# Performance work log

Hardware: AMD Instinct MI355X
Metric: run time of the kernel (lower is better)

Reference implementation:

```python
import jax, jax.numpy as jnp
import numpy as np

N_HEADS = 8
EPS = 1e-6


def setup_inputs() -> dict:
    key = jax.random.key(0)
    k1, k2, k3, k4, k5 = jax.random.split(key, 5)
    C_in, C_out = 512, 512
    x = jax.random.normal(k1, (4, C_in, 128, 128), dtype=jnp.float32)
    # Linear layers: torch stores weight as (out, in); init ~ U(-1/sqrt(in), 1/sqrt(in))
    s_in = 1.0 / np.sqrt(C_in)
    w_qkv = jax.random.uniform(k2, (3 * C_in, C_in), minval=-s_in, maxval=s_in, dtype=jnp.float32)
    b_qkv = jax.random.uniform(k3, (3 * C_in,), minval=-s_in, maxval=s_in, dtype=jnp.float32)
    w_out = jax.random.uniform(k4, (C_out, C_in), minval=-s_in, maxval=s_in, dtype=jnp.float32)
    b_out = jax.random.uniform(k5, (C_out,), minval=-s_in, maxval=s_in, dtype=jnp.float32)
    return {"x": x, "w_qkv": w_qkv, "b_qkv": b_qkv, "w_out": w_out, "b_out": b_out}


def reference(x, w_qkv, b_qkv, w_out, b_out):
    B, C = x.shape[0], x.shape[1]
    spatial = x.shape[2:]
    c = C // N_HEADS  # channels per head
    # features_last=False: move channels to last, flatten spatial -> (B, N, C)
    xl = jnp.moveaxis(x, 1, -1).reshape(B, -1, C)
    N = xl.shape[1]
    qkv = xl @ w_qkv.T + b_qkv  # (B, N, 3*C)
    # einops '(qkv head channels)': qkv outermost, then head, then channels
    qkv = qkv.reshape(B, N, 3, N_HEADS, c)
    q = jax.nn.relu(qkv[:, :, 0])  # (B, N, H, c)
    k = jax.nn.relu(qkv[:, :, 1])
    v = qkv[:, :, 2]
    # Associativity: value @ key^T @ query == value @ (key^T @ query).
    # kq[b,h,c,d] = sum_n k[b,n,h,c] * q[b,n,h,d]  -> small (c x c) per head
    kq = jnp.einsum('bnhc,bnhd->bhcd', k, q)
    vkq = jnp.einsum('bnhc,bhcd->bnhd', v, kq)  # (B, N, H, c)
    # Padded ones-row of value corresponds to column-sum of kq over axis c
    norm = kq.sum(axis=2)[:, None] + EPS  # (B, 1, H, c)
    attn = vkq / norm  # (B, N, H, c)
    # torch: (B,H,N,c).moveaxis(1,-1) -> (B,N,c,H); flatten(-2) -> (B,N,c*H)
    attn = jnp.transpose(attn, (0, 1, 3, 2)).reshape(B, N, -1)
    out = attn @ w_out.T + b_out  # (B, N, C_out)
    out = out.reshape(B, *spatial, -1)
    out = jnp.moveaxis(out, -1, 1)  # (B, C_out, *spatial)
    return out
```

## Files before the change

### kernel.cpp

```cpp
#include <hip/hip_runtime.h>
#include <hip/hip_bf16.h>
#include <stdint.h>

#define NSP 16384
#define BATCH 4
#define EPSV 1e-6f

typedef __attribute__((ext_vector_type(8))) short fragAB;
typedef __attribute__((ext_vector_type(4))) float fragC;

__device__ __forceinline__ unsigned short f2bf(float f) {
    union { float f; unsigned u; } un; un.f = f;
    unsigned r = un.u + 0x7fffu + ((un.u >> 16) & 1u);
    return (unsigned short)(r >> 16);
}

#define GLD_LDS(g, l) __builtin_amdgcn_global_load_lds( \
    (const __attribute__((address_space(1))) void*)(g), \
    (__attribute__((address_space(3))) void*)(l), 16, 0, 0)

__device__ __forceinline__ fragAB ldfrag(const unsigned short* ls, int m, int g) {
    return *(const fragAB*)&ls[((m >> 3) << 9) + ((m & 7) << 6) + ((g ^ (m & 7)) << 3)];
}

__global__ __launch_bounds__(256) void transpose_x(const float* __restrict__ x,
                                                   unsigned short* __restrict__ xt) {
    __shared__ float lds[64 * 65];
    const int b  = blockIdx.z;
    const int c0 = blockIdx.y * 64;
    const int n0 = blockIdx.x * 64;
    const int t  = threadIdx.x;
    const int nl = (t & 15) * 4;
    const int cl = t >> 4;
#pragma unroll
    for (int i = 0; i < 4; ++i) {
        int c = cl + i * 16;
        float4 v = *(const float4*)&x[((size_t)(b * 512 + c0 + c)) * NSP + n0 + nl];
        float* row = &lds[c * 65 + nl];
        row[0] = v.x; row[1] = v.y; row[2] = v.z; row[3] = v.w;
    }
    __syncthreads();
#pragma unroll
    for (int i = 0; i < 2; ++i) {
        int ch = t + i * 256;
        int n  = ch >> 3;
        int co = (ch & 7) * 8;
        unsigned v0, v1, v2, v3;
        v0 = f2bf(lds[(co + 0) * 65 + n]) | ((unsigned)f2bf(lds[(co + 1) * 65 + n]) << 16);
        v1 = f2bf(lds[(co + 2) * 65 + n]) | ((unsigned)f2bf(lds[(co + 3) * 65 + n]) << 16);
        v2 = f2bf(lds[(co + 4) * 65 + n]) | ((unsigned)f2bf(lds[(co + 5) * 65 + n]) << 16);
        v3 = f2bf(lds[(co + 6) * 65 + n]) | ((unsigned)f2bf(lds[(co + 7) * 65 + n]) << 16);
        uint4 pk; pk.x = v0; pk.y = v1; pk.z = v2; pk.w = v3;
        *(uint4*)&xt[((size_t)(b * NSP + n0 + n)) * 512 + c0 + co] = pk;
    }
}

__global__ __launch_bounds__(256) void prep(const float* __restrict__ wqkv,
                                            unsigned short* __restrict__ wqb,
                                            unsigned short* __restrict__ wvT) {
    __shared__ float lds[64 * 65];
    const int blk = blockIdx.x;
    const int t   = threadIdx.x;
    if (blk < 512) {
        int i = (blk * 256 + t) * 4;
        float4 v = *(const float4*)&wqkv[i];
        uint2 pk;
        pk.x = f2bf(v.x) | ((unsigned)f2bf(v.y) << 16);
        pk.y = f2bf(v.z) | ((unsigned)f2bf(v.w) << 16);
        *(uint2*)&wqb[i] = pk;
        return;
    }
    const int c0  = ((blk - 512) & 7) * 64;
    const int ch0 = ((blk - 512) >> 3) * 64;
    const int cl  = (t & 15) * 4;
    const int rl  = t >> 4;
#pragma unroll
    for (int i = 0; i < 4; ++i) {
        int r = rl + i * 16;
        float4 v = *(const float4*)&wqkv[((size_t)(1024 + ch0 + r)) * 512 + c0 + cl];
        float* row = &lds[r * 65 + cl];
        row[0] = v.x; row[1] = v.y; row[2] = v.z; row[3] = v.w;
    }
    __syncthreads();
#pragma unroll
    for (int i = 0; i < 2; ++i) {
        int idx = t + i * 256;
        int c = idx >> 3;
        int g = (idx & 7) * 8;
        unsigned v0, v1, v2, v3;
        v0 = f2bf(lds[(g + 0) * 65 + c]) | ((unsigned)f2bf(lds[(g + 1) * 65 + c]) << 16);
        v1 = f2bf(lds[(g + 2) * 65 + c]) | ((unsigned)f2bf(lds[(g + 3) * 65 + c]) << 16);
        v2 = f2bf(lds[(g + 4) * 65 + c]) | ((unsigned)f2bf(lds[(g + 5) * 65 + c]) << 16);
        v3 = f2bf(lds[(g + 6) * 65 + c]) | ((unsigned)f2bf(lds[(g + 7) * 65 + c]) << 16);
        uint4 pk; pk.x = v0; pk.y = v1; pk.z = v2; pk.w = v3;
        *(uint4*)&wvT[((size_t)(c0 + c)) * 512 + ch0 + g] = pk;
    }
}

__global__ __launch_bounds__(256, 2) void gemm_qkv(
    const unsigned short* __restrict__ xt, const unsigned short* __restrict__ wq,
    const float* __restrict__ bqkv,
    unsigned short* __restrict__ qbuf, unsigned short* __restrict__ kbuf) {
    __shared__ unsigned short Als[128 * 64];
    __shared__ unsigned short Bls[256 * 64];
    const int b  = blockIdx.z;
    const int n0 = blockIdx.x * 128;
    const int j0 = blockIdx.y * 256;
    const int t  = threadIdx.x;
    const int wv = t >> 6, ln = t & 63;
    const unsigned short* Ag = xt + (size_t)(b * NSP + n0) * 512;
    const unsigned short* Bg = wq + (size_t)j0 * 512;

    fragC acc[8][4];
#pragma unroll
    for (int i = 0; i < 8; ++i)
#pragma unroll
        for (int j = 0; j < 4; ++j) { acc[i][j][0]=0.f; acc[i][j][1]=0.f; acc[i][j][2]=0.f; acc[i][j][3]=0.f; }

    const int srow = ln >> 3;
    const int scol = ((ln & 7) ^ srow) << 3;

    for (int k0 = 0; k0 < 512; k0 += 64) {
#pragma unroll
        for (int i = 0; i < 4; ++i) {
            int ca = wv * 4 + i;
            GLD_LDS(Ag + (size_t)(ca * 8 + srow) * 512 + k0 + scol, &Als[ca * 512]);
        }
#pragma unroll
        for (int i = 0; i < 8; ++i) {
            int cb = wv * 8 + i;
            GLD_LDS(Bg + (size_t)(cb * 8 + srow) * 512 + k0 + scol, &Bls[cb * 512]);
        }
        __syncthreads();
#pragma unroll
        for (int kk = 0; kk < 64; kk += 32) {
            int g = (kk >> 3) + (ln >> 4);
            fragAB bf[4];
#pragma unroll
            for (int nt = 0; nt < 4; ++nt) bf[nt] = ldfrag(Bls, wv * 64 + nt * 16 + (ln & 15), g);
#pragma unroll
            for (int mt = 0; mt < 8; ++mt) {
                fragAB a = ldfrag(Als, mt * 16 + (ln & 15), g);
#pragma unroll
                for (int nt = 0; nt < 4; ++nt)
                    acc[mt][nt] = __builtin_amdgcn_mfma_f32_16x16x32_bf16(a, bf[nt], acc[mt][nt], 0, 0, 0);
            }
        }
        __syncthreads();
    }

    unsigned short* dst = (j0 < 512 ? qbuf : kbuf) + (size_t)b * 512 * NSP;
#pragma unroll
    for (int nt = 0; nt < 4; ++nt) {
        int j  = j0 + wv * 64 + nt * 16 + (ln & 15);
        int ch = j & 511;
        float bias = bqkv[j];
#pragma unroll
        for (int mt = 0; mt < 8; ++mt) {
            int n = n0 + mt * 16 + (ln >> 4) * 4;
            float r0 = acc[mt][nt][0] + bias; r0 = r0 > 0.f ? r0 : 0.f;
            float r1 = acc[mt][nt][1] + bias; r1 = r1 > 0.f ? r1 : 0.f;
            float r2 = acc[mt][nt][2] + bias; r2 = r2 > 0.f ? r2 : 0.f;
            float r3 = acc[mt][nt][3] + bias; r3 = r3 > 0.f ? r3 : 0.f;
            uint2 pk;
            pk.x = f2bf(r0) | ((unsigned)f2bf(r1) << 16);
            pk.y = f2bf(r2) | ((unsigned)f2bf(r3) << 16);
            *(uint2*)&dst[(size_t)ch * NSP + n] = pk;
        }
    }
}

__global__ __launch_bounds__(256) void kq_kernel(
    const unsigned short* __restrict__ kbuf, const unsigned short* __restrict__ qbuf,
    float* __restrict__ kq) {
    __shared__ unsigned short Kls[64 * 64];
    __shared__ unsigned short Qls[64 * 64];
    const int bh = blockIdx.x;
    const int chn = blockIdx.y;
    const int t = threadIdx.x, wv = t >> 6, ln = t & 63;
    const unsigned short* Kg = kbuf + (size_t)(bh * 64) * NSP;
    const unsigned short* Qg = qbuf + (size_t)(bh * 64) * NSP;
    fragC acc[4];
#pragma unroll
    for (int i = 0; i < 4; ++i) { acc[i][0]=0.f; acc[i][1]=0.f; acc[i][2]=0.f; acc[i][3]=0.f; }
    const int srow = ln >> 3;
    const int scol = ((ln & 7) ^ srow) << 3;
    const int mA = wv * 16 + (ln & 15);
    const int nbeg = chn * 1024;
    for (int nb = nbeg; nb < nbeg + 1024; nb += 64) {
#pragma unroll
        for (int i = 0; i < 2; ++i) {
            int chunk = wv * 2 + i;
            int row = chunk * 8 + srow;
            GLD_LDS(Kg + (size_t)row * NSP + nb + scol, &Kls[chunk * 512]);
            GLD_LDS(Qg + (size_t)row * NSP + nb + scol, &Qls[chunk * 512]);
        }
        __syncthreads();
#pragma unroll
        for (int kk = 0; kk < 64; kk += 32) {
            int g = (kk >> 3) + (ln >> 4);
            fragAB a = ldfrag(Kls, mA, g);
#pragma unroll
            for (int dt = 0; dt < 4; ++dt) {
                fragAB bq = ldfrag(Qls, dt * 16 + (ln & 15), g);
                acc[dt] = __builtin_amdgcn_mfma_f32_16x16x32_bf16(a, bq, acc[dt], 0, 0, 0);
            }
        }
        __syncthreads();
    }
    float* kqb = kq + bh * 4096;
#pragma unroll
    for (int dt = 0; dt < 4; ++dt) {
        int d = dt * 16 + (ln & 15);
#pragma unroll
        for (int r = 0; r < 4; ++r) {
            int c = wv * 16 + (ln >> 4) * 4 + r;
            atomicAdd(&kqb[c * 64 + d], acc[dt][r]);
        }
    }
}

__global__ __launch_bounds__(256) void w2_kernel(
    const float* __restrict__ kq, const float* __restrict__ wout,
    const float* __restrict__ bqkv,
    unsigned short* __restrict__ W2, float* __restrict__ bias2acc) {
    __shared__ float slab[64 * 65];
    __shared__ float part[4 * 64];
    __shared__ float rnorm[64];
    __shared__ float wsc[32 * 65];
    const int jc = blockIdx.x;
    const int h  = blockIdx.y;
    const int b  = blockIdx.z;
    const int t  = threadIdx.x;
    const float* kqb = kq + ((size_t)(b * 8 + h)) * 4096;
#pragma unroll
    for (int i = 0; i < 4; ++i) {
        int e = t * 16 + i * 4;
        float4 v = *(const float4*)&kqb[e];
        float* r = &slab[(e >> 6) * 65 + (e & 63)];
        r[0] = v.x; r[1] = v.y; r[2] = v.z; r[3] = v.w;
    }
    __syncthreads();
    {
        int d = t & 63, cq = t >> 6;
        float s = 0.f;
        for (int c = cq * 16; c < cq * 16 + 16; ++c) s += slab[c * 65 + d];
        part[cq * 64 + d] = s;
    }
    __syncthreads();
    if (t < 64) rnorm[t] = 1.0f / (part[t] + part[64 + t] + part[128 + t] + part[192 + t] + EPSV);
    __syncthreads();
    {
        int jl = t >> 3;
        const float* wrow = &wout[((size_t)(jc * 32 + jl)) * 512 + h];
#pragma unroll
        for (int i = 0; i < 8; ++i) {
            int d = (t & 7) * 8 + i;
            wsc[jl * 65 + d] = wrow[d * 8] * rnorm[d];
        }
    }
    __syncthreads();
    {
        int jl = t >> 3, cg = (t & 7) * 8;
        int j  = jc * 32 + jl;
        float a[8] = {0.f, 0.f, 0.f, 0.f, 0.f, 0.f, 0.f, 0.f};
        for (int d = 0; d < 64; ++d) {
            float w = wsc[jl * 65 + d];
#pragma unroll
            for (int i = 0; i < 8; ++i) a[i] += w * slab[(cg + i) * 65 + d];
        }
        uint4 pk;
        pk.x = f2bf(a[0]) | ((unsigned)f2bf(a[1]) << 16);
        pk.y = f2bf(a[2]) | ((unsigned)f2bf(a[3]) << 16);
        pk.z = f2bf(a[4]) | ((unsigned)f2bf(a[5]) << 16);
        pk.w = f2bf(a[6]) | ((unsigned)f2bf(a[7]) << 16);
        *(uint4*)&W2[((size_t)(b * 512 + j)) * 512 + h * 64 + cg] = pk;
        const float* bv = &bqkv[1024 + h * 64 + cg];
        float p = 0.f;
#pragma unroll
        for (int i = 0; i < 8; ++i) p += a[i] * bv[i];
        p += __shfl_down(p, 4, 64);
        p += __shfl_down(p, 2, 64);
        p += __shfl_down(p, 1, 64);
        if ((t & 7) == 0) atomicAdd(&bias2acc[b * 512 + j], p);
    }
}

__global__ __launch_bounds__(256) void w3_kernel(
    const unsigned short* __restrict__ wvT, const unsigned short* __restrict__ W2,
    unsigned short* __restrict__ W3) {
    __shared__ unsigned short Als[128 * 64];
    __shared__ unsigned short Bls[128 * 64];
    const int b  = blockIdx.z;
    const int m0 = blockIdx.x * 128;
    const int n0 = blockIdx.y * 128;
    const int t  = threadIdx.x;
    const int wv = t >> 6, ln = t & 63;
    const unsigned short* Ag = wvT + (size_t)m0 * 512;
    const unsigned short* Bg = W2 + ((size_t)(b * 512 + n0)) * 512;

    fragC acc[4][4];
#pragma unroll
    for (int i = 0; i < 4; ++i)
#pragma unroll
        for (int j = 0; j < 4; ++j) { acc[i][j][0]=0.f; acc[i][j][1]=0.f; acc[i][j][2]=0.f; acc[i][j][3]=0.f; }

    const int mw = (wv >> 1) * 64, nw = (wv & 1) * 64;
    const int srow = ln >> 3;
    const int scol = ((ln & 7) ^ srow) << 3;

    for (int k0 = 0; k0 < 512; k0 += 64) {
#pragma unroll
        for (int i = 0; i < 4; ++i) {
            int chunk = wv * 4 + i;
            int row = chunk * 8 + srow;
            GLD_LDS(Ag + (size_t)row * 512 + k0 + scol, &Als[chunk * 512]);
            GLD_LDS(Bg + (size_t)row * 512 + k0 + scol, &Bls[chunk * 512]);
        }
        __syncthreads();
#pragma unroll
        for (int kk = 0; kk < 64; kk += 32) {
            int g = (kk >> 3) + (ln >> 4);
            fragAB a[4], bf[4];
#pragma unroll
            for (int mt = 0; mt < 4; ++mt) a[mt]  = ldfrag(Als, mw + mt * 16 + (ln & 15), g);
#pragma unroll
            for (int nt = 0; nt < 4; ++nt) bf[nt] = ldfrag(Bls, nw + nt * 16 + (ln & 15), g);
#pragma unroll
            for (int mt = 0; mt < 4; ++mt)
#pragma unroll
                for (int nt = 0; nt < 4; ++nt)
                    acc[mt][nt] = __builtin_amdgcn_mfma_f32_16x16x32_bf16(a[mt], bf[nt], acc[mt][nt], 0, 0, 0);
        }
        __syncthreads();
    }

#pragma unroll
    for (int mt = 0; mt < 4; ++mt)
#pragma unroll
        for (int nt = 0; nt < 4; ++nt) {
            int c = m0 + mw + mt * 16 + (ln >> 4) * 4;
            int j = n0 + nw + nt * 16 + (ln & 15);
            uint2 pk;
            pk.x = f2bf(acc[mt][nt][0]) | ((unsigned)f2bf(acc[mt][nt][1]) << 16);
            pk.y = f2bf(acc[mt][nt][2]) | ((unsigned)f2bf(acc[mt][nt][3]) << 16);
            *(uint2*)&W3[((size_t)(b * 512 + j)) * 512 + c] = pk;
        }
}

__global__ __launch_bounds__(256, 2) void gemm_out(
    const unsigned short* __restrict__ xt, const unsigned short* __restrict__ W3,
    const float* __restrict__ bias2acc, const float* __restrict__ bout,
    float* __restrict__ out) {
    __shared__ unsigned short Als[128 * 64];
    __shared__ unsigned short Bls[256 * 64];
    const int b  = blockIdx.z;
    const int n0 = blockIdx.x * 128;
    const int j0 = blockIdx.y * 256;
    const int t  = threadIdx.x;
    const int wv = t >> 6, ln = t & 63;
    const unsigned short* Ag = xt + (size_t)(b * NSP + n0) * 512;
    const unsigned short* Bg = W3 + ((size_t)(b * 512 + j0)) * 512;

    fragC acc[8][4];
#pragma unroll
    for (int i = 0; i < 8; ++i)
#pragma unroll
        for (int j = 0; j < 4; ++j) { acc[i][j][0]=0.f; acc[i][j][1]=0.f; acc[i][j][2]=0.f; acc[i][j][3]=0.f; }

    const int srow = ln >> 3;
    const int scol = ((ln & 7) ^ srow) << 3;

    for (int k0 = 0; k0 < 512; k0 += 64) {
#pragma unroll
        for (int i = 0; i < 4; ++i) {
            int ca = wv * 4 + i;
            GLD_LDS(Ag + (size_t)(ca * 8 + srow) * 512 + k0 + scol, &Als[ca * 512]);
        }
#pragma unroll
        for (int i = 0; i < 8; ++i) {
            int cb = wv * 8 + i;
            GLD_LDS(Bg + (size_t)(cb * 8 + srow) * 512 + k0 + scol, &Bls[cb * 512]);
        }
        __syncthreads();
#pragma unroll
        for (int kk = 0; kk < 64; kk += 32) {
            int g = (kk >> 3) + (ln >> 4);
            fragAB bf[4];
#pragma unroll
            for (int nt = 0; nt < 4; ++nt) bf[nt] = ldfrag(Bls, wv * 64 + nt * 16 + (ln & 15), g);
#pragma unroll
            for (int mt = 0; mt < 8; ++mt) {
                fragAB a = ldfrag(Als, mt * 16 + (ln & 15), g);
#pragma unroll
                for (int nt = 0; nt < 4; ++nt)
                    acc[mt][nt] = __builtin_amdgcn_mfma_f32_16x16x32_bf16(a, bf[nt], acc[mt][nt], 0, 0, 0);
            }
        }
        __syncthreads();
    }

#pragma unroll
    for (int nt = 0; nt < 4; ++nt) {
        int j = j0 + wv * 64 + nt * 16 + (ln & 15);
        float bias = bout[j] + bias2acc[b * 512 + j];
#pragma unroll
        for (int mt = 0; mt < 8; ++mt) {
            int n = n0 + mt * 16 + (ln >> 4) * 4;
            float4 v;
            v.x = acc[mt][nt][0] + bias;
            v.y = acc[mt][nt][1] + bias;
            v.z = acc[mt][nt][2] + bias;
            v.w = acc[mt][nt][3] + bias;
            *(float4*)&out[((size_t)(b * 512 + j)) * NSP + n] = v;
        }
    }
}

extern "C" void kernel_launch(void* const* d_in, const int* in_sizes, int n_in,
                              void* d_out, int out_size, void* d_ws, size_t ws_size,
                              hipStream_t stream) {
    const float* x    = (const float*)d_in[0];
    const float* wqkv = (const float*)d_in[1];
    const float* bqkv = (const float*)d_in[2];
    const float* wout = (const float*)d_in[3];
    const float* bout = (const float*)d_in[4];
    float* out = (float*)d_out;

    char* p = (char*)d_ws;
    unsigned short* xt   = (unsigned short*)p; p += (size_t)BATCH * NSP * 512 * 2;
    unsigned short* wqb  = (unsigned short*)p; p += (size_t)1024 * 512 * 2;
    unsigned short* wvT  = (unsigned short*)p; p += (size_t)512 * 512 * 2;
    unsigned short* qbuf = (unsigned short*)p; p += (size_t)BATCH * 512 * NSP * 2;
    unsigned short* kbuf = (unsigned short*)p; p += (size_t)BATCH * 512 * NSP * 2;
    float*          kq   = (float*)p;          p += (size_t)BATCH * 32768 * 4;
    float*          b2a  = (float*)p;          p += (size_t)BATCH * 512 * 4;
    unsigned short* W2   = (unsigned short*)p; p += (size_t)BATCH * 512 * 512 * 2;
    unsigned short* W3   = (unsigned short*)p; p += (size_t)BATCH * 512 * 512 * 2;

    hipMemsetAsync(kq, 0, (size_t)BATCH * 32768 * 4 + (size_t)BATCH * 512 * 4, stream);
    transpose_x<<<dim3(256, 8, BATCH), 256, 0, stream>>>(x, xt);
    prep<<<dim3(576), 256, 0, stream>>>(wqkv, wqb, wvT);
    gemm_qkv<<<dim3(128, 4, BATCH), 256, 0, stream>>>(xt, wqb, bqkv, qbuf, kbuf);
    kq_kernel<<<dim3(32, 16), 256, 0, stream>>>(kbuf, qbuf, kq);
    w2_kernel<<<dim3(16, 8, BATCH), 256, 0, stream>>>(kq, wout, bqkv, W2, b2a);
    w3_kernel<<<dim3(4, 4, BATCH), 256, 0, stream>>>(wvT, W2, W3);
    gemm_out<<<dim3(128, 2, BATCH), 256, 0, stream>>>(xt, W3, b2a, bout, out);
}
```

Before: 435.8 us.

## Fuse Q/K projection GEMM with per-head K^T Q reduction in LDS

Merges the QKV projection GEMM and the kq reduction kernel into one kernel. Each block computes Q and K for two heads over a 128-token tile, stages the relu'd bf16 results in LDS, and immediately accumulates K^T Q into the global kq buffer with atomics. This removes the write and re-read of the full Q and K buffers through global memory, plus one launch. In exchange the grid drops to 512 blocks, each re-reading its x tile four times, and the kernel issues many more atomics and uses more LDS, which may lower occupancy.

```diff
diff --git a/kernel.cpp b/kernel.cpp
--- a/kernel.cpp
+++ b/kernel.cpp
@@ -21,6 +21,10 @@
 
 __device__ __forceinline__ fragAB ldfrag(const unsigned short* ls, int m, int g) {
     return *(const fragAB*)&ls[((m >> 3) << 9) + ((m & 7) << 6) + ((g ^ (m & 7)) << 3)];
+}
+
+__device__ __forceinline__ int tidx(int ch, int g) {
+    return (ch << 7) + ((g ^ (ch & 7)) << 3);
 }
 
 __global__ __launch_bounds__(256) void transpose_x(const float* __restrict__ x,
@@ -97,126 +101,120 @@
     }
 }
 
-__global__ __launch_bounds__(256, 2) void gemm_qkv(
+__global__ __launch_bounds__(256, 2) void gemm_qk_kq(
     const unsigned short* __restrict__ xt, const unsigned short* __restrict__ wq,
-    const float* __restrict__ bqkv,
-    unsigned short* __restrict__ qbuf, unsigned short* __restrict__ kbuf) {
-    __shared__ unsigned short Als[128 * 64];
-    __shared__ unsigned short Bls[256 * 64];
+    const float* __restrict__ bqkv, float* __restrict__ kq) {
+    __shared__ unsigned short S[(128 + 256) * 64];
+    __shared__ unsigned short Qt[128 * 128];
+    unsigned short* Bls = &S[8192];
+    unsigned short* Kt  = &S[0];
+
     const int b  = blockIdx.z;
     const int n0 = blockIdx.x * 128;
-    const int j0 = blockIdx.y * 256;
     const int t  = threadIdx.x;
     const int wv = t >> 6, ln = t & 63;
+    const int wm = wv >> 1, wn = wv & 1;
     const unsigned short* Ag = xt + (size_t)(b * NSP + n0) * 512;
-    const unsigned short* Bg = wq + (size_t)j0 * 512;
-
-    fragC acc[8][4];
-#pragma unroll
-    for (int i = 0; i < 8; ++i)
-#pragma unroll
-        for (int j = 0; j < 4; ++j) { acc[i][j][0]=0.f; acc[i][j][1]=0.f; acc[i][j][2]=0.f; acc[i][j][3]=0.f; }
-
     const int srow = ln >> 3;
     const int scol = ((ln & 7) ^ srow) << 3;
 
-    for (int k0 = 0; k0 < 512; k0 += 64) {
-#pragma unroll
-        for (int i = 0; i < 4; ++i) {
-            int ca = wv * 4 + i;
-            GLD_LDS(Ag + (size_t)(ca * 8 + srow) * 512 + k0 + scol, &Als[ca * 512]);
-        }
-#pragma unroll
-        for (int i = 0; i < 8; ++i) {
-            int cb = wv * 8 + i;
-            GLD_LDS(Bg + (size_t)(cb * 8 + srow) * 512 + k0 + scol, &Bls[cb * 512]);
-        }
-        __syncthreads();
-#pragma unroll
-        for (int kk = 0; kk < 64; kk += 32) {
-            int g = (kk >> 3) + (ln >> 4);
-            fragAB bf[4];
-#pragma unroll
-            for (int nt = 0; nt < 4; ++nt) bf[nt] = ldfrag(Bls, wv * 64 + nt * 16 + (ln & 15), g);
-#pragma unroll
-            for (int mt = 0; mt < 8; ++mt) {
-                fragAB a = ldfrag(Als, mt * 16 + (ln & 15), g);
-#pragma unroll
-                for (int nt = 0; nt < 4; ++nt)
-                    acc[mt][nt] = __builtin_amdgcn_mfma_f32_16x16x32_bf16(a, bf[nt], acc[mt][nt], 0, 0, 0);
-            }
-        }
-        __syncthreads();
-    }
-
-    unsigned short* dst = (j0 < 512 ? qbuf : kbuf) + (size_t)b * 512 * NSP;
-#pragma unroll
-    for (int nt = 0; nt < 4; ++nt) {
-        int j  = j0 + wv * 64 + nt * 16 + (ln & 15);
-        int ch = j & 511;
-        float bias = bqkv[j];
-#pragma unroll
-        for (int mt = 0; mt < 8; ++mt) {
-            int n = n0 + mt * 16 + (ln >> 4) * 4;
-            float r0 = acc[mt][nt][0] + bias; r0 = r0 > 0.f ? r0 : 0.f;
-            float r1 = acc[mt][nt][1] + bias; r1 = r1 > 0.f ? r1 : 0.f;
-            float r2 = acc[mt][nt][2] + bias; r2 = r2 > 0.f ? r2 : 0.f;
-            float r3 = acc[mt][nt][3] + bias; r3 = r3 > 0.f ? r3 : 0.f;
-            uint2 pk;
-            pk.x = f2bf(r0) | ((unsigned)f2bf(r1) << 16);
-            pk.y = f2bf(r2) | ((unsigned)f2bf(r3) << 16);
-            *(uint2*)&dst[(size_t)ch * NSP + n] = pk;
-        }
-    }
-}
-
-__global__ __launch_bounds__(256) void kq_kernel(
-    const unsigned short* __restrict__ kbuf, const unsigned short* __restrict__ qbuf,
-    float* __restrict__ kq) {
-    __shared__ unsigned short Kls[64 * 64];
-    __shared__ unsigned short Qls[64 * 64];
-    const int bh = blockIdx.x;
-    const int chn = blockIdx.y;
-    const int t = threadIdx.x, wv = t >> 6, ln = t & 63;
-    const unsigned short* Kg = kbuf + (size_t)(bh * 64) * NSP;
-    const unsigned short* Qg = qbuf + (size_t)(bh * 64) * NSP;
-    fragC acc[4];
-#pragma unroll
-    for (int i = 0; i < 4; ++i) { acc[i][0]=0.f; acc[i][1]=0.f; acc[i][2]=0.f; acc[i][3]=0.f; }
-    const int srow = ln >> 3;
-    const int scol = ((ln & 7) ^ srow) << 3;
-    const int mA = wv * 16 + (ln & 15);
-    const int nbeg = chn * 1024;
-    for (int nb = nbeg; nb < nbeg + 1024; nb += 64) {
-#pragma unroll
-        for (int i = 0; i < 2; ++i) {
-            int chunk = wv * 2 + i;
-            int row = chunk * 8 + srow;
-            GLD_LDS(Kg + (size_t)row * NSP + nb + scol, &Kls[chunk * 512]);
-            GLD_LDS(Qg + (size_t)row * NSP + nb + scol, &Qls[chunk * 512]);
-        }
-        __syncthreads();
-#pragma unroll
-        for (int kk = 0; kk < 64; kk += 32) {
-            int g = (kk >> 3) + (ln >> 4);
-            fragAB a = ldfrag(Kls, mA, g);
-#pragma unroll
-            for (int dt = 0; dt < 4; ++dt) {
-                fragAB bq = ldfrag(Qls, dt * 16 + (ln & 15), g);
-                acc[dt] = __builtin_amdgcn_mfma_f32_16x16x32_bf16(a, bq, acc[dt], 0, 0, 0);
-            }
-        }
-        __syncthreads();
-    }
-    float* kqb = kq + bh * 4096;
-#pragma unroll
-    for (int dt = 0; dt < 4; ++dt) {
-        int d = dt * 16 + (ln & 15);
-#pragma unroll
-        for (int r = 0; r < 4; ++r) {
-            int c = wv * 16 + (ln >> 4) * 4 + r;
-            atomicAdd(&kqb[c * 64 + d], acc[dt][r]);
-        }
+    for (int hc = 0; hc < 4; ++hc) {
+        fragC acc[4][8];
+#pragma unroll
+        for (int i = 0; i < 4; ++i)
+#pragma unroll
+            for (int j = 0; j < 8; ++j) { acc[i][j][0]=0.f; acc[i][j][1]=0.f; acc[i][j][2]=0.f; acc[i][j][3]=0.f; }
+
+        for (int k0 = 0; k0 < 512; k0 += 64) {
+#pragma unroll
+            for (int i = 0; i < 4; ++i) {
+                int ca = wv * 4 + i;
+                GLD_LDS(Ag + (size_t)(ca * 8 + srow) * 512 + k0 + scol, &S[ca * 512]);
+            }
+#pragma unroll
+            for (int i = 0; i < 8; ++i) {
+                int cb = wv * 8 + i;
+                int jl = cb * 8 + srow;
+                int rg = hc * 128 + jl + ((jl & 128) ? 384 : 0);
+                GLD_LDS(wq + (size_t)rg * 512 + k0 + scol, &Bls[cb * 512]);
+            }
+            __syncthreads();
+#pragma unroll
+            for (int kk = 0; kk < 64; kk += 32) {
+                int g = (kk >> 3) + (ln >> 4);
+                fragAB bf[8];
+#pragma unroll
+                for (int nt = 0; nt < 8; ++nt) bf[nt] = ldfrag(Bls, wn * 128 + nt * 16 + (ln & 15), g);
+#pragma unroll
+                for (int mt = 0; mt < 4; ++mt) {
+                    fragAB a = ldfrag(S, wm * 64 + mt * 16 + (ln & 15), g);
+#pragma unroll
+                    for (int nt = 0; nt < 8; ++nt)
+                        acc[mt][nt] = __builtin_amdgcn_mfma_f32_16x16x32_bf16(a, bf[nt], acc[mt][nt], 0, 0, 0);
+                }
+            }
+            __syncthreads();
+        }
+
+        {
+            unsigned short* T = wn ? Kt : Qt;
+#pragma unroll
+            for (int nt = 0; nt < 8; ++nt) {
+                int chl = nt * 16 + (ln & 15);
+                float bias = bqkv[hc * 128 + chl + (wn ? 512 : 0)];
+#pragma unroll
+                for (int mt = 0; mt < 4; ++mt) {
+                    int nb = wm * 64 + mt * 16 + (ln >> 4) * 4;
+                    float r0 = acc[mt][nt][0] + bias; r0 = r0 > 0.f ? r0 : 0.f;
+                    float r1 = acc[mt][nt][1] + bias; r1 = r1 > 0.f ? r1 : 0.f;
+                    float r2 = acc[mt][nt][2] + bias; r2 = r2 > 0.f ? r2 : 0.f;
+                    float r3 = acc[mt][nt][3] + bias; r3 = r3 > 0.f ? r3 : 0.f;
+                    uint2 pk;
+                    pk.x = f2bf(r0) | ((unsigned)f2bf(r1) << 16);
+                    pk.y = f2bf(r2) | ((unsigned)f2bf(r3) << 16);
+                    int g = nb >> 3, o = nb & 7;
+                    *(uint2*)&T[tidx(chl, g) + o] = pk;
+                }
+            }
+        }
+        __syncthreads();
+
+        {
+            fragC ak[4][2];
+#pragma unroll
+            for (int i = 0; i < 4; ++i)
+#pragma unroll
+                for (int j = 0; j < 2; ++j) { ak[i][j][0]=0.f; ak[i][j][1]=0.f; ak[i][j][2]=0.f; ak[i][j][3]=0.f; }
+            const int dh = wn * 32;
+#pragma unroll
+            for (int kk = 0; kk < 128; kk += 32) {
+                int g = (kk >> 3) + (ln >> 4);
+                fragAB bq[2];
+#pragma unroll
+                for (int dt = 0; dt < 2; ++dt)
+                    bq[dt] = *(const fragAB*)&Qt[tidx(wm * 64 + dh + dt * 16 + (ln & 15), g)];
+#pragma unroll
+                for (int mt = 0; mt < 4; ++mt) {
+                    fragAB a = *(const fragAB*)&Kt[tidx(wm * 64 + mt * 16 + (ln & 15), g)];
+#pragma unroll
+                    for (int dt = 0; dt < 2; ++dt)
+                        ak[mt][dt] = __builtin_amdgcn_mfma_f32_16x16x32_bf16(a, bq[dt], ak[mt][dt], 0, 0, 0);
+                }
+            }
+            float* kqb = kq + ((size_t)(b * 8 + hc * 2 + wm)) * 4096;
+#pragma unroll
+            for (int mt = 0; mt < 4; ++mt)
+#pragma unroll
+                for (int dt = 0; dt < 2; ++dt) {
+                    int d = dh + dt * 16 + (ln & 15);
+#pragma unroll
+                    for (int r = 0; r < 4; ++r) {
+                        int c = mt * 16 + (ln >> 4) * 4 + r;
+                        atomicAdd(&kqb[c * 64 + d], ak[mt][dt][r]);
+                    }
+                }
+        }
+        __syncthreads();
     }
 }
 
@@ -431,8 +429,6 @@
     unsigned short* xt   = (unsigned short*)p; p += (size_t)BATCH * NSP * 512 * 2;
     unsigned short* wqb  = (unsigned short*)p; p += (size_t)1024 * 512 * 2;
     unsigned short* wvT  = (unsigned short*)p; p += (size_t)512 * 512 * 2;
-    unsigned short* qbuf = (unsigned short*)p; p += (size_t)BATCH * 512 * NSP * 2;
-    unsigned short* kbuf = (unsigned short*)p; p += (size_t)BATCH * 512 * NSP * 2;
     float*          kq   = (float*)p;          p += (size_t)BATCH * 32768 * 4;
     float*          b2a  = (float*)p;          p += (size_t)BATCH * 512 * 4;
     unsigned short* W2   = (unsigned short*)p; p += (size_t)BATCH * 512 * 512 * 2;
@@ -441,8 +437,7 @@
     hipMemsetAsync(kq, 0, (size_t)BATCH * 32768 * 4 + (size_t)BATCH * 512 * 4, stream);
     transpose_x<<<dim3(256, 8, BATCH), 256, 0, stream>>>(x, xt);
     prep<<<dim3(576), 256, 0, stream>>>(wqkv, wqb, wvT);
-    gemm_qkv<<<dim3(128, 4, BATCH), 256, 0, stream>>>(xt, wqb, bqkv, qbuf, kbuf);
-    kq_kernel<<<dim3(32, 16), 256, 0, stream>>>(kbuf, qbuf, kq);
+    gemm_qk_kq<<<dim3(128, 1, BATCH), 256, 0, stream>>>(xt, wqb, bqkv, kq);
     w2_kernel<<<dim3(16, 8, BATCH), 256, 0, stream>>>(kq, wout, bqkv, W2, b2a);
     w3_kernel<<<dim3(4, 4, BATCH), 256, 0, stream>>>(wvT, W2, W3);
     gemm_out<<<dim3(128, 2, BATCH), 256, 0, stream>>>(xt, W3, b2a, bout, out);
```

Result: slower. 447.9 us (+2.8%).
